# Kernel optimization log

Hardware: AMD Instinct MI355X
Metric: run time of the kernel (lower is better)

## Reference

```python
import jax, jax.numpy as jnp
import numpy as np

N, D = 2048, 32


def setup_inputs() -> dict:
    key = jax.random.key(0)
    k1, k2, k3, k4 = jax.random.split(key, 4)
    x = jax.random.normal(k1, (N, D), dtype=jnp.float32)
    # positive hyperparameters (Gamma-prior samples in the original)
    lengthscale = jax.random.uniform(k2, (D,), dtype=jnp.float32, minval=0.5, maxval=2.0)
    alpha = jax.random.uniform(k3, (), dtype=jnp.float32, minval=0.5, maxval=2.0)
    outputscale = jax.random.uniform(k4, (), dtype=jnp.float32, minval=0.5, maxval=2.0)
    return {"x": x, "lengthscale": lengthscale, "alpha": alpha, "outputscale": outputscale}


def reference(x, lengthscale, alpha, outputscale):
    # Additive RQ kernel: k(xi, xj) = outputscale * sum_d (1 + ((xi_d - xj_d)/l_d)^2 / (2*alpha))^(-alpha)
    xs = x / lengthscale                      # [N, D]
    d2 = (xs[:, None, :] - xs[None, :, :]) ** 2   # [N, N, D] per-dim squared distance
    covar = outputscale * jnp.sum((1.0 + d2 / (2.0 * alpha)) ** (-alpha), axis=-1)  # [N, N]
    mean = jnp.zeros((x.shape[0],), dtype=x.dtype)  # ZeroMean
    return mean, covar
```

## Files before the change

### kernel.cpp

```cpp
#include <hip/hip_runtime.h>


#define D 32
#define TILE 32

#if __has_builtin(__builtin_amdgcn_exp2f)
#define EXP2F(x) __builtin_amdgcn_exp2f(x)
#else
#define EXP2F(x) exp2f(x)
#endif
#if __has_builtin(__builtin_amdgcn_logf)
#define LOG2F(x) __builtin_amdgcn_logf(x)
#else
#define LOG2F(x) __log2f(x)
#endif

__global__ __launch_bounds__(256) void rq_covar_sym_kernel(
    const float* __restrict__ x,
    const float* __restrict__ ls,
    const float* __restrict__ alpha_p,
    const float* __restrict__ os_p,
    float* __restrict__ mean_out,
    float* __restrict__ covar,
    int n, int ntiles)
{
    __shared__ float As[TILE][36];
    __shared__ float Bs[TILE][36];
    __shared__ float pow2tab[160];

    const int t = threadIdx.x;
    const int k = blockIdx.x;

    {
        const int idx = k * 256 + t;
        if (idx < n) mean_out[idx] = 0.0f;
    }

    const float nt = (float)ntiles;
    int bi = (int)(nt + 0.5f - sqrtf((nt + 0.5f) * (nt + 0.5f) - 2.0f * (float)k));
    while (bi > 0 && k < bi * ntiles - (bi * (bi - 1)) / 2) --bi;
    while (k >= (bi + 1) * ntiles - ((bi + 1) * bi) / 2) ++bi;
    const int bj = bi + (k - (bi * ntiles - (bi * (bi - 1)) / 2));

    const float alpha = alpha_p[0];
    const float oscale = os_p[0];
    const float nalpha = -alpha;
    const float rs2a = rsqrtf(2.0f * alpha);

    for (int e = t; e < 160; e += 256)
        pow2tab[e] = EXP2F(nalpha * (float)(e - 127));

    const float Xc[8] = {1.990393f, 1.915735f, 1.777785f, 1.597545f,
                         1.402455f, 1.222215f, 1.084265f, 1.009607f};
    float dd[8];
#pragma unroll
    for (int i = 0; i < 8; ++i)
        dd[i] = EXP2F(nalpha * LOG2F(Xc[i]));
#pragma unroll
    for (int j = 1; j < 8; ++j) {
#pragma unroll
        for (int i = 7; i >= 1; --i) {
            if (i >= j)
                dd[i] = (dd[i] - dd[i - 1]) * (1.0f / (Xc[i] - Xc[i - j]));
        }
    }
    float C[8] = {0.0f, 0.0f, 0.0f, 0.0f, 0.0f, 0.0f, 0.0f, 0.0f};
    C[0] = dd[7];
#pragma unroll
    for (int i = 6; i >= 0; --i) {
        const float yi = Xc[i] - 1.5f;
#pragma unroll
        for (int kk = 7; kk >= 1; --kk)
            C[kk] = fmaf(-yi, C[kk], C[kk - 1]);
        C[0] = fmaf(-yi, C[0], dd[i]);
    }

    {
        const int row = t >> 3;
        const int q = (t & 7) * 4;
        const float4 lv = *reinterpret_cast<const float4*>(&ls[q]);
        const float4 a = *reinterpret_cast<const float4*>(&x[(size_t)(bi * TILE + row) * D + q]);
        const float4 b = *reinterpret_cast<const float4*>(&x[(size_t)(bj * TILE + row) * D + q]);
        const float w0 = rs2a / lv.x, w1 = rs2a / lv.y, w2 = rs2a / lv.z, w3 = rs2a / lv.w;
        As[row][q + 0] = a.x * w0;  Bs[row][q + 0] = b.x * w0;
        As[row][q + 1] = a.y * w1;  Bs[row][q + 1] = b.y * w1;
        As[row][q + 2] = a.z * w2;  Bs[row][q + 2] = b.z * w2;
        As[row][q + 3] = a.w * w3;  Bs[row][q + 3] = b.w * w3;
    }
    __syncthreads();

    const int c = t & 31;
    const int r0 = t >> 5;

    float bs[D];
#pragma unroll
    for (int q = 0; q < D; q += 4) {
        const float4 v = *reinterpret_cast<const float4*>(&Bs[c][q]);
        bs[q] = v.x; bs[q + 1] = v.y; bs[q + 2] = v.z; bs[q + 3] = v.w;
    }

    float acc[4];
#pragma unroll
    for (int kk = 0; kk < 4; ++kk) {
        const int r = r0 + kk * 8;
        float as[D];
#pragma unroll
        for (int q = 0; q < D; q += 4) {
            const float4 v = *reinterpret_cast<const float4*>(&As[r][q]);
            as[q] = v.x; as[q + 1] = v.y; as[q + 2] = v.z; as[q + 3] = v.w;
        }
        float s0 = 0.0f, s1 = 0.0f, s2 = 0.0f, s3 = 0.0f;
#pragma unroll
        for (int d = 0; d < D; d += 4) {
#pragma unroll
            for (int j = 0; j < 4; ++j) {
                const float diff = as[d + j] - bs[d + j];
                const float tv = fmaf(diff, diff, 1.0f);
                const unsigned bits = __float_as_uint(tv);
                const float pw = pow2tab[bits >> 23];
                const float m = __uint_as_float((bits & 0x7FFFFFu) | 0x3F800000u);
                const float sm = m - 1.5f;
                float p = fmaf(C[7], sm, C[6]);
                p = fmaf(p, sm, C[5]);
                p = fmaf(p, sm, C[4]);
                p = fmaf(p, sm, C[3]);
                p = fmaf(p, sm, C[2]);
                p = fmaf(p, sm, C[1]);
                p = fmaf(p, sm, C[0]);
                const float term_pw = pw;
                if (j == 0) s0 = fmaf(p, term_pw, s0);
                else if (j == 1) s1 = fmaf(p, term_pw, s1);
                else if (j == 2) s2 = fmaf(p, term_pw, s2);
                else s3 = fmaf(p, term_pw, s3);
            }
        }
        acc[kk] = oscale * ((s0 + s1) + (s2 + s3));
    }

#pragma unroll
    for (int kk = 0; kk < 4; ++kk) {
        const int r = r0 + kk * 8;
        covar[(size_t)(bi * TILE + r) * n + (bj * TILE + c)] = acc[kk];
    }

    if (bi != bj) {
        __syncthreads();
#pragma unroll
        for (int kk = 0; kk < 4; ++kk) {
            As[r0 + kk * 8][c] = acc[kk];
        }
        __syncthreads();
#pragma unroll
        for (int kk = 0; kk < 4; ++kk) {
            const int rr = r0 + kk * 8;
            const float v = As[c][rr];
            covar[(size_t)(bj * TILE + rr) * n + (bi * TILE + c)] = v;
        }
    }
}

extern "C" void kernel_launch(void* const* d_in, const int* in_sizes, int n_in,
                              void* d_out, int out_size, void* d_ws, size_t ws_size,
                              hipStream_t stream) {
    const float* x = (const float*)d_in[0];
    const float* ls = (const float*)d_in[1];
    const float* alpha_p = (const float*)d_in[2];
    const float* os_p = (const float*)d_in[3];

    const int n = in_sizes[0] / D;
    const int ntiles = n / TILE;
    const int nblocks = ntiles * (ntiles + 1) / 2;

    float* mean_out = (float*)d_out;
    float* covar = (float*)d_out + n;

    rq_covar_sym_kernel<<<nblocks, 256, 0, stream>>>(x, ls, alpha_p, os_p,
                                                     mean_out, covar, n, ntiles);
}
```

Baseline: 85.71 us.

## Load B rows into registers directly, drop center shift, raise occupancy hint

Each thread now reads its B row straight from global memory into registers and scales it there, which removes the Bs shared tile and its staging loads. The polynomial is rebuilt around zero instead of 1.5, so the per-element subtraction is gone, at some cost to conditioning. A rows are streamed from shared memory as float4 inside the d-loop rather than held in a full register array, and launch_bounds asks for 4 blocks per CU to raise occupancy. Risks include more register pressure or spilling under the tighter bound, slightly lower polynomial accuracy, and the global B reads being uncoalesced.

```diff
diff --git a/kernel.cpp b/kernel.cpp
--- a/kernel.cpp
+++ b/kernel.cpp
@@ -15,7 +15,7 @@
 #define LOG2F(x) __log2f(x)
 #endif
 
-__global__ __launch_bounds__(256) void rq_covar_sym_kernel(
+__global__ __launch_bounds__(256, 4) void rq_covar_sym_kernel(
     const float* __restrict__ x,
     const float* __restrict__ ls,
     const float* __restrict__ alpha_p,
@@ -25,7 +25,6 @@
     int n, int ntiles)
 {
     __shared__ float As[TILE][36];
-    __shared__ float Bs[TILE][36];
     __shared__ float pow2tab[160];
 
     const int t = threadIdx.x;
@@ -50,6 +49,22 @@
     for (int e = t; e < 160; e += 256)
         pow2tab[e] = EXP2F(nalpha * (float)(e - 127));
 
+    const int c = t & 31;
+    const int r0 = t >> 5;
+    float bs[D];
+    {
+        const float* bp = x + (size_t)(bj * TILE + c) * D;
+#pragma unroll
+        for (int q = 0; q < D; q += 4) {
+            const float4 bv = *reinterpret_cast<const float4*>(bp + q);
+            const float4 lv = *reinterpret_cast<const float4*>(ls + q);
+            bs[q + 0] = bv.x * (rs2a / lv.x);
+            bs[q + 1] = bv.y * (rs2a / lv.y);
+            bs[q + 2] = bv.z * (rs2a / lv.z);
+            bs[q + 3] = bv.w * (rs2a / lv.w);
+        }
+    }
+
     const float Xc[8] = {1.990393f, 1.915735f, 1.777785f, 1.597545f,
                          1.402455f, 1.222215f, 1.084265f, 1.009607f};
     float dd[8];
@@ -68,7 +83,7 @@
     C[0] = dd[7];
 #pragma unroll
     for (int i = 6; i >= 0; --i) {
-        const float yi = Xc[i] - 1.5f;
+        const float yi = Xc[i];
 #pragma unroll
         for (int kk = 7; kk >= 1; --kk)
             C[kk] = fmaf(-yi, C[kk], C[kk - 1]);
@@ -80,58 +95,40 @@
         const int q = (t & 7) * 4;
         const float4 lv = *reinterpret_cast<const float4*>(&ls[q]);
         const float4 a = *reinterpret_cast<const float4*>(&x[(size_t)(bi * TILE + row) * D + q]);
-        const float4 b = *reinterpret_cast<const float4*>(&x[(size_t)(bj * TILE + row) * D + q]);
-        const float w0 = rs2a / lv.x, w1 = rs2a / lv.y, w2 = rs2a / lv.z, w3 = rs2a / lv.w;
-        As[row][q + 0] = a.x * w0;  Bs[row][q + 0] = b.x * w0;
-        As[row][q + 1] = a.y * w1;  Bs[row][q + 1] = b.y * w1;
-        As[row][q + 2] = a.z * w2;  Bs[row][q + 2] = b.z * w2;
-        As[row][q + 3] = a.w * w3;  Bs[row][q + 3] = b.w * w3;
+        As[row][q + 0] = a.x * (rs2a / lv.x);
+        As[row][q + 1] = a.y * (rs2a / lv.y);
+        As[row][q + 2] = a.z * (rs2a / lv.z);
+        As[row][q + 3] = a.w * (rs2a / lv.w);
     }
     __syncthreads();
-
-    const int c = t & 31;
-    const int r0 = t >> 5;
-
-    float bs[D];
-#pragma unroll
-    for (int q = 0; q < D; q += 4) {
-        const float4 v = *reinterpret_cast<const float4*>(&Bs[c][q]);
-        bs[q] = v.x; bs[q + 1] = v.y; bs[q + 2] = v.z; bs[q + 3] = v.w;
-    }
 
     float acc[4];
 #pragma unroll
     for (int kk = 0; kk < 4; ++kk) {
         const int r = r0 + kk * 8;
-        float as[D];
-#pragma unroll
-        for (int q = 0; q < D; q += 4) {
-            const float4 v = *reinterpret_cast<const float4*>(&As[r][q]);
-            as[q] = v.x; as[q + 1] = v.y; as[q + 2] = v.z; as[q + 3] = v.w;
-        }
         float s0 = 0.0f, s1 = 0.0f, s2 = 0.0f, s3 = 0.0f;
 #pragma unroll
         for (int d = 0; d < D; d += 4) {
+            const float4 av = *reinterpret_cast<const float4*>(&As[r][d]);
 #pragma unroll
             for (int j = 0; j < 4; ++j) {
-                const float diff = as[d + j] - bs[d + j];
+                const float a_j = (j == 0) ? av.x : (j == 1) ? av.y : (j == 2) ? av.z : av.w;
+                const float diff = a_j - bs[d + j];
                 const float tv = fmaf(diff, diff, 1.0f);
                 const unsigned bits = __float_as_uint(tv);
                 const float pw = pow2tab[bits >> 23];
                 const float m = __uint_as_float((bits & 0x7FFFFFu) | 0x3F800000u);
-                const float sm = m - 1.5f;
-                float p = fmaf(C[7], sm, C[6]);
-                p = fmaf(p, sm, C[5]);
-                p = fmaf(p, sm, C[4]);
-                p = fmaf(p, sm, C[3]);
-                p = fmaf(p, sm, C[2]);
-                p = fmaf(p, sm, C[1]);
-                p = fmaf(p, sm, C[0]);
-                const float term_pw = pw;
-                if (j == 0) s0 = fmaf(p, term_pw, s0);
-                else if (j == 1) s1 = fmaf(p, term_pw, s1);
-                else if (j == 2) s2 = fmaf(p, term_pw, s2);
-                else s3 = fmaf(p, term_pw, s3);
+                float p = fmaf(C[7], m, C[6]);
+                p = fmaf(p, m, C[5]);
+                p = fmaf(p, m, C[4]);
+                p = fmaf(p, m, C[3]);
+                p = fmaf(p, m, C[2]);
+                p = fmaf(p, m, C[1]);
+                p = fmaf(p, m, C[0]);
+                if (j == 0) s0 = fmaf(p, pw, s0);
+                else if (j == 1) s1 = fmaf(p, pw, s1);
+                else if (j == 2) s2 = fmaf(p, pw, s2);
+                else s3 = fmaf(p, pw, s3);
             }
         }
         acc[kk] = oscale * ((s0 + s1) + (s2 + s3));
```

Result: slower. 90.00 us (+5.0%).
